# Kernel tuning notes

Hardware: AMD Instinct MI355X
Metric: run time of the kernel (lower is better)

Reference implementation:

```python
import jax, jax.numpy as jnp
import numpy as np

N_NODES = 50000
N_EDGES = 800000
D_IN = 128
HC = 128
D_OUT = 128
BN_EPS = 1e-5
RRELU_SLOPE = (1.0 / 8.0 + 1.0 / 3.0) / 2.0  # RReLU eval mode: (lower+upper)/2 = 11/48


def setup_inputs() -> dict:
    key = jax.random.key(0)
    ks = jax.random.split(key, 10)
    s_in = 1.0 / np.sqrt(D_IN)
    s_hc = 1.0 / np.sqrt(HC)
    return {
        "x": jax.random.normal(ks[0], (N_NODES, D_IN), jnp.float32),
        "edge_index": jax.random.randint(ks[1], (2, N_EDGES), 0, N_NODES),
        "edge_attr": jax.random.uniform(ks[2], (N_EDGES,), jnp.float32),
        # conv1: GraphConv(D_IN -> HC): lin_rel (with bias) + lin_root (no bias)
        "W1_rel": jax.random.normal(ks[3], (HC, D_IN), jnp.float32) * s_in,
        "b1": jnp.zeros((HC,), jnp.float32),
        "W1_root": jax.random.normal(ks[4], (HC, D_IN), jnp.float32) * s_in,
        # bn1 affine params
        "gamma": jnp.ones((HC,), jnp.float32),
        "beta": jnp.zeros((HC,), jnp.float32),
        # conv2: GraphConv(HC -> D_OUT)
        "W2_rel": jax.random.normal(ks[5], (D_OUT, HC), jnp.float32) * s_hc,
        "b2": jnp.zeros((D_OUT,), jnp.float32),
        "W2_root": jax.random.normal(ks[6], (D_OUT, HC), jnp.float32) * s_hc,
    }


def graph_conv(x, src, tgt, edge_w, W_rel, b_rel, W_root):
    # message: edge_weight * x[src]; aggregate: scatter-add into target nodes
    msg = x[src] * edge_w[:, None]                                   # [E, F]
    agg = jax.ops.segment_sum(msg, tgt, num_segments=x.shape[0])     # [N, F]
    return agg @ W_rel.T + b_rel + x @ W_root.T                      # [N, F_out]


def reference(x, edge_index, edge_attr, W1_rel, b1, W1_root, gamma, beta, W2_rel, b2, W2_root):
    src, tgt = edge_index[0], edge_index[1]
    h = graph_conv(x, src, tgt, edge_attr, W1_rel, b1, W1_root)      # [N, HC]
    # BatchNorm1d (training mode: biased batch stats over node dim)
    mean = h.mean(axis=0)
    var = h.var(axis=0)
    h = (h - mean) * jax.lax.rsqrt(var + BN_EPS) * gamma + beta
    # RReLU (deterministic eval slope)
    h = jnp.where(h >= 0, h, h * RRELU_SLOPE)
    return graph_conv(h, src, tgt, edge_attr, W2_rel, b2, W2_root)   # [N, D_OUT]
```

## Files before the change

### kernel.cpp

```cpp
#include <hip/hip_runtime.h>

#define N_NODES 50000
#define N_EDGES 800000
#define F 128
#define BN_EPS 1e-5f
#define SLOPE 0.22916666666666666f

#define NBKT 196
#define BKT_CAP 8192
#define P1_CHUNK 4096
#define P1_EPB 16
#define P1_BLKS 196
#define CASTX_BLKS 6250
#define CASTW_BLKS 64
#define BKT_FINAL_CAP 9984
#define REC_CAP 1160192
#define N_RT 3125
#define NPART 8

typedef __attribute__((ext_vector_type(8))) short bf16x8;
typedef __attribute__((ext_vector_type(4))) float f32x4;
typedef unsigned long long u64;

__device__ __forceinline__ float bf2f(ushort u) {
    union { uint i; float f; } v; v.i = (uint)u << 16; return v.f;
}
__device__ __forceinline__ ushort f2bf(float f) {
    union { float f; uint i; } v; v.f = f;
    uint r = v.i + 0x7fffu + ((v.i >> 16) & 1u);
    return (ushort)(r >> 16);
}
__device__ __forceinline__ uint cvtpk(float lo, float hi) {
    uint r;
    asm("v_cvt_pk_bf16_f32 %0, %1, %2" : "=v"(r) : "v"(lo), "v"(hi));
    return r;
}

__global__ __launch_bounds__(256) void s1p_k(const int* __restrict__ src,
        const int* __restrict__ tgt, const float* __restrict__ ew,
        int* __restrict__ bcur, u64* __restrict__ stg,
        const float* __restrict__ x, ushort* __restrict__ xb,
        const float* __restrict__ W1r, const float* __restrict__ W1t,
        const float* __restrict__ W2r, const float* __restrict__ W2t,
        ushort* __restrict__ wb) {
    const int b = blockIdx.x;
    if (b >= P1_BLKS) {
        if (b < P1_BLKS + CASTX_BLKS) {
            int i = (b - P1_BLKS) * 256 + threadIdx.x;
            float4 v = reinterpret_cast<const float4*>(x)[i];
            ushort4 o;
            o.x = f2bf(v.x); o.y = f2bf(v.y); o.z = f2bf(v.z); o.w = f2bf(v.w);
            reinterpret_cast<ushort4*>(xb)[i] = o;
        } else {
            int i = (b - P1_BLKS - CASTX_BLKS) * 256 + threadIdx.x;
            int m = i >> 12;
            int j = i & 4095;
            const float* sp = (m == 0) ? W1r : (m == 1) ? W1t : (m == 2) ? W2r : W2t;
            float4 v = reinterpret_cast<const float4*>(sp)[j];
            ushort4 o;
            o.x = f2bf(v.x); o.y = f2bf(v.y); o.z = f2bf(v.z); o.w = f2bf(v.w);
            reinterpret_cast<ushort4*>(wb)[i] = o;
        }
        return;
    }
    __shared__ uint cnt[256];
    __shared__ uint base[256];
    __shared__ uint lcur[256];
    __shared__ uint gbase[256];
    __shared__ u64 lrec[P1_CHUNK];

    const int e0 = b * P1_CHUNK;
    const int nE = min(P1_CHUNK, N_EDGES - e0);
    cnt[threadIdx.x] = 0;
    __syncthreads();

    u64 myrec[P1_EPB];
    bool myok[P1_EPB];
#pragma unroll
    for (int k = 0; k < P1_EPB; ++k) {
        int idx = threadIdx.x + (k << 8);
        bool ok = idx < nE;
        myok[k] = ok;
        if (ok) {
            int e = e0 + idx;
            uint t = (uint)tgt[e];
            uint lo = (uint)(ushort)src[e] | ((uint)f2bf(ew[e]) << 16);
            myrec[k] = (u64)lo | ((u64)t << 32);
            atomicAdd(&cnt[t >> 8], 1u);
        }
    }
    __syncthreads();
    uint v = cnt[threadIdx.x];
    base[threadIdx.x] = v;
    __syncthreads();
    for (int o = 1; o < 256; o <<= 1) {
        uint t = (threadIdx.x >= (unsigned)o) ? base[threadIdx.x - o] : 0;
        __syncthreads();
        base[threadIdx.x] += t;
        __syncthreads();
    }
    uint excl = base[threadIdx.x] - v;
    base[threadIdx.x] = excl;
    lcur[threadIdx.x] = excl;
    if (threadIdx.x < NBKT && v > 0)
        gbase[threadIdx.x] = (uint)threadIdx.x * BKT_CAP +
                             (uint)atomicAdd(&bcur[threadIdx.x], (int)v);
    __syncthreads();
#pragma unroll
    for (int k = 0; k < P1_EPB; ++k) {
        if (myok[k]) {
            uint bb = (uint)(myrec[k] >> 40);
            uint slot = atomicAdd(&lcur[bb], 1u);
            lrec[slot] = myrec[k];
        }
    }
    __syncthreads();
    for (int s = threadIdx.x; s < nE; s += 256) {
        u64 r = lrec[s];
        uint bb = (uint)(r >> 40);
        stg[gbase[bb] + ((uint)s - base[bb])] = r;
    }
}

__global__ __launch_bounds__(256) void sort2_k(const int* __restrict__ bcur,
        const u64* __restrict__ stg, uint* __restrict__ recs, int2* __restrict__ rng) {
    __shared__ int lcnt[256];
    __shared__ int lcur[256];
    __shared__ int sc[256];
    __shared__ int fbase_s;
    __shared__ uint lrec[BKT_FINAL_CAP];
    const int b = blockIdx.x;
    const int tid = threadIdx.x;

    int cnt_t = (tid < NBKT) ? bcur[tid] : 0;
    int stride_t = (tid < NBKT) ? (((cnt_t + 7) & ~7) + 1792) : 0;
    sc[tid] = stride_t;
    lcnt[tid] = 0;
    __syncthreads();
    for (int o = 1; o < 256; o <<= 1) {
        int t = (tid >= o) ? sc[tid - o] : 0;
        __syncthreads();
        sc[tid] += t;
        __syncthreads();
    }
    if (tid == b) fbase_s = sc[tid] - stride_t;
    __syncthreads();
    const int fbase = fbase_s;
    const int cnt = bcur[b];
    const u64* sb = stg + (size_t)b * BKT_CAP;

    for (int i = tid; i < cnt; i += 256)
        atomicAdd(&lcnt[(int)(sb[i] >> 32) & 255], 1);
    __syncthreads();
    const int node = b * 256 + tid;
    int myc = lcnt[tid];
    int myp = (myc + 7) & ~7;
    if (node >= N_NODES) myp = 0;
    sc[tid] = myp;
    __syncthreads();
    for (int o = 1; o < 256; o <<= 1) {
        int t = (tid >= o) ? sc[tid - o] : 0;
        __syncthreads();
        sc[tid] += t;
        __syncthreads();
    }
    const int myoff = sc[tid] - myp;
    const int ptot = sc[255];
    lcur[tid] = myoff;
    if (node < N_NODES) rng[node] = make_int2(fbase + myoff, fbase + myoff + myp);
    for (int i = tid; i < ptot; i += 256) lrec[i] = 0;
    __syncthreads();
    for (int i = tid; i < cnt; i += 256) {
        u64 r = sb[i];
        int n = (int)(r >> 32) & 255;
        int p = atomicAdd(&lcur[n], 1);
        lrec[p] = (uint)r;
    }
    __syncthreads();
    for (int i = tid; i < ptot; i += 256) recs[fbase + i] = lrec[i];
}

__device__ __forceinline__ void fma8(float* a, uint4 u, float w) {
    a[0] = fmaf(w, __uint_as_float(u.x << 16), a[0]);
    a[1] = fmaf(w, __uint_as_float(u.x & 0xffff0000u), a[1]);
    a[2] = fmaf(w, __uint_as_float(u.y << 16), a[2]);
    a[3] = fmaf(w, __uint_as_float(u.y & 0xffff0000u), a[3]);
    a[4] = fmaf(w, __uint_as_float(u.z << 16), a[4]);
    a[5] = fmaf(w, __uint_as_float(u.z & 0xffff0000u), a[5]);
    a[6] = fmaf(w, __uint_as_float(u.w << 16), a[6]);
    a[7] = fmaf(w, __uint_as_float(u.w & 0xffff0000u), a[7]);
}

template <int LAYER>
__global__ __launch_bounds__(256) void fused_k(
        const ushort* __restrict__ featb, const int2* __restrict__ rng,
        const uint* __restrict__ recs, const ushort* __restrict__ Wr,
        const ushort* __restrict__ Wt, const float* __restrict__ bias,
        float* __restrict__ Sp, float* __restrict__ S2p,
        ushort* __restrict__ outh, float* __restrict__ outf) {
    __shared__ __align__(16) uint aggu[16 * 64];

    const int tid = threadIdx.x;
    const int lane = tid & 63;
    const int wave = tid >> 6;
    const int row0 = blockIdx.x * 16;
    const int quad = lane >> 4;
    const int l16 = lane & 15;
    const uint fbyte = (uint)l16 << 4;
    const int qq = quad * 2;
    const char* fb = (const char*)featb;

#pragma unroll
    for (int i = 0; i < 4; ++i) {
        const int r = wave * 4 + i;
        const int2 rr = rng[row0 + r];
        float a[8] = {0.f, 0.f, 0.f, 0.f, 0.f, 0.f, 0.f, 0.f};
        for (int p = rr.x; p < rr.y; p += 8) {
            uint2 rc = *reinterpret_cast<const uint2*>(recs + p + qq);
            uint4 u0 = *reinterpret_cast<const uint4*>(fb + (((rc.x & 0xffffu) << 8) + fbyte));
            uint4 u1 = *reinterpret_cast<const uint4*>(fb + (((rc.y & 0xffffu) << 8) + fbyte));
            fma8(a, u0, __uint_as_float(rc.x & 0xffff0000u));
            fma8(a, u1, __uint_as_float(rc.y & 0xffff0000u));
        }
#pragma unroll
        for (int j = 0; j < 8; ++j) {
            a[j] += __shfl_xor(a[j], 16);
            a[j] += __shfl_xor(a[j], 32);
        }
        uint o0 = cvtpk(a[0], a[1]);
        uint o1 = cvtpk(a[2], a[3]);
        uint o2 = cvtpk(a[4], a[5]);
        uint o3 = cvtpk(a[6], a[7]);
        if (lane < 16) {
            const int idx = ((r * 64) + (l16 << 2)) ^ ((r & 7) << 2);
            *reinterpret_cast<uint4*>(&aggu[idx]) = make_uint4(o0, o1, o2, o3);
        }
    }
    __syncthreads();

    const int cb = wave * 32;
    const float bias0 = bias[cb + l16];
    const float bias1 = bias[cb + 16 + l16];

    f32x4 acc0 = {0.f, 0.f, 0.f, 0.f};
    f32x4 acc1 = {0.f, 0.f, 0.f, 0.f};

#pragma unroll
    for (int s = 0; s < 4; ++s) {
        const int k0 = s * 32 + quad * 8;
        const int ai = (l16 * 64 + (k0 >> 1)) ^ ((l16 & 7) << 2);
        bf16x8 aR = *reinterpret_cast<const bf16x8*>(&aggu[ai]);
        bf16x8 w0 = *reinterpret_cast<const bf16x8*>(Wr + (cb + l16) * F + k0);
        bf16x8 w1 = *reinterpret_cast<const bf16x8*>(Wr + (cb + 16 + l16) * F + k0);
        acc0 = __builtin_amdgcn_mfma_f32_16x16x32_bf16(aR, w0, acc0, 0, 0, 0);
        acc1 = __builtin_amdgcn_mfma_f32_16x16x32_bf16(aR, w1, acc1, 0, 0, 0);
    }
#pragma unroll
    for (int s = 0; s < 4; ++s) {
        const int k0 = s * 32 + quad * 8;
        bf16x8 aT = *reinterpret_cast<const bf16x8*>(featb + (size_t)(row0 + l16) * F + k0);
        bf16x8 w0 = *reinterpret_cast<const bf16x8*>(Wt + (cb + l16) * F + k0);
        bf16x8 w1 = *reinterpret_cast<const bf16x8*>(Wt + (cb + 16 + l16) * F + k0);
        acc0 = __builtin_amdgcn_mfma_f32_16x16x32_bf16(aT, w0, acc0, 0, 0, 0);
        acc1 = __builtin_amdgcn_mfma_f32_16x16x32_bf16(aT, w1, acc1, 0, 0, 0);
    }

    const int rbase = row0 + quad * 4;
    if (LAYER == 1) {
        float s0 = 0.f, q0 = 0.f, s1 = 0.f, q1 = 0.f;
#pragma unroll
        for (int g = 0; g < 4; ++g) {
            float v0 = acc0[g] + bias0;
            float v1 = acc1[g] + bias1;
            outh[(size_t)(rbase + g) * F + cb + l16] = f2bf(v0);
            outh[(size_t)(rbase + g) * F + cb + 16 + l16] = f2bf(v1);
            s0 += v0; q0 += v0 * v0;
            s1 += v1; q1 += v1 * v1;
        }
        s0 += __shfl_down(s0, 32); s0 += __shfl_down(s0, 16);
        q0 += __shfl_down(q0, 32); q0 += __shfl_down(q0, 16);
        s1 += __shfl_down(s1, 32); s1 += __shfl_down(s1, 16);
        q1 += __shfl_down(q1, 32); q1 += __shfl_down(q1, 16);
        if (lane < 16) {
            float* Sb = Sp + (size_t)(blockIdx.x & (NPART - 1)) * 128;
            float* S2b = S2p + (size_t)(blockIdx.x & (NPART - 1)) * 128;
            unsafeAtomicAdd(&Sb[cb + lane], s0);
            unsafeAtomicAdd(&S2b[cb + lane], q0);
            unsafeAtomicAdd(&Sb[cb + 16 + lane], s1);
            unsafeAtomicAdd(&S2b[cb + 16 + lane], q1);
        }
    } else {
#pragma unroll
        for (int g = 0; g < 4; ++g) {
            outf[(size_t)(rbase + g) * F + cb + l16] = acc0[g] + bias0;
            outf[(size_t)(rbase + g) * F + cb + 16 + l16] = acc1[g] + bias1;
        }
    }
}

__global__ __launch_bounds__(256) void norm_act_k(const ushort* __restrict__ hraw,
        const float* __restrict__ Sp, const float* __restrict__ S2p,
        const float* __restrict__ gamma, const float* __restrict__ beta,
        ushort* __restrict__ hb) {
    __shared__ float sc_s[128], sh_s[128];
    if (threadIdx.x < 128) {
        int j = threadIdx.x;
        float s = 0.f, q = 0.f;
#pragma unroll
        for (int p = 0; p < NPART; ++p) {
            s += Sp[p * 128 + j];
            q += S2p[p * 128 + j];
        }
        float mean = s * (1.f / N_NODES);
        float var = q * (1.f / N_NODES) - mean * mean;
        float inv = rsqrtf(var + BN_EPS);
        float sc = gamma[j] * inv;
        sc_s[j] = sc;
        sh_s[j] = beta[j] - mean * sc;
    }
    __syncthreads();
    int i = blockIdx.x * 256 + threadIdx.x;
    int cbase = (i & 31) * 4;
    uint2 u = reinterpret_cast<const uint2*>(hraw)[i];
    float4 v = make_float4(bf2f((ushort)u.x), bf2f((ushort)(u.x >> 16)),
                           bf2f((ushort)u.y), bf2f((ushort)(u.y >> 16)));
    float4 sc = *reinterpret_cast<const float4*>(&sc_s[cbase]);
    float4 sh = *reinterpret_cast<const float4*>(&sh_s[cbase]);
    v.x = v.x * sc.x + sh.x;
    v.y = v.y * sc.y + sh.y;
    v.z = v.z * sc.z + sh.z;
    v.w = v.w * sc.w + sh.w;
    v.x = v.x >= 0.f ? v.x : v.x * SLOPE;
    v.y = v.y >= 0.f ? v.y : v.y * SLOPE;
    v.z = v.z >= 0.f ? v.z : v.z * SLOPE;
    v.w = v.w >= 0.f ? v.w : v.w * SLOPE;
    uint2 o;
    o.x = cvtpk(v.x, v.y);
    o.y = cvtpk(v.z, v.w);
    reinterpret_cast<uint2*>(hb)[i] = o;
}

extern "C" void kernel_launch(void* const* d_in, const int* in_sizes, int n_in,
                              void* d_out, int out_size, void* d_ws, size_t ws_size,
                              hipStream_t stream) {
    const float* x     = (const float*)d_in[0];
    const int*   ei    = (const int*)d_in[1];
    const float* ea    = (const float*)d_in[2];
    const float* W1r   = (const float*)d_in[3];
    const float* b1    = (const float*)d_in[4];
    const float* W1t   = (const float*)d_in[5];
    const float* gamma = (const float*)d_in[6];
    const float* beta  = (const float*)d_in[7];
    const float* W2r   = (const float*)d_in[8];
    const float* b2    = (const float*)d_in[9];
    const float* W2t   = (const float*)d_in[10];
    float* out = (float*)d_out;

    char* ws = (char*)d_ws;
    size_t off = 0;
    u64*    stg   = (u64*)(ws + off);    off += (size_t)NBKT * BKT_CAP * 8;
    ushort* featb = (ushort*)(ws + off); off += (size_t)N_NODES * F * 2;
    uint*   recs  = (uint*)(ws + off);   off += (size_t)REC_CAP * 4;
    int*    bcur  = (int*)(ws + off);    off += 256 * 4;
    float*  Sp    = (float*)(ws + off);  off += NPART * 128 * 4;
    float*  S2p   = (float*)(ws + off);  off += NPART * 128 * 4;
    int2*   rng   = (int2*)(ws + off);   off += (size_t)N_NODES * 8;
    ushort* wb    = (ushort*)(ws + off); off += 4 * 16384 * 2;
    ushort* hraw  = (ushort*)stg;

    const int* srcp = ei;
    const int* tgtp = ei + N_EDGES;

    hipMemsetAsync(bcur, 0, 256 * 4 + 2 * NPART * 128 * 4, stream);
    s1p_k<<<P1_BLKS + CASTX_BLKS + CASTW_BLKS, 256, 0, stream>>>(
        srcp, tgtp, ea, bcur, stg, x, featb, W1r, W1t, W2r, W2t, wb);
    sort2_k<<<NBKT, 256, 0, stream>>>(bcur, stg, recs, rng);

    fused_k<1><<<N_RT, 256, 0, stream>>>(featb, rng, recs, wb, wb + 16384, b1,
                                         Sp, S2p, hraw, out);
    norm_act_k<<<CASTX_BLKS, 256, 0, stream>>>(hraw, Sp, S2p, gamma, beta, featb);
    fused_k<2><<<N_RT, 256, 0, stream>>>(featb, rng, recs, wb + 32768, wb + 49152, b2,
                                         Sp, S2p, hraw, out);
}
```

Baseline: 254.8 us.

## Replace two-level bucket sort with global histogram/scan/atomic scatter CSR and interleave gather rows

Replaces the two-pass bucketed edge sort with a plain CSR build: a global per-node degree histogram, a single-block scan that computes padded row ranges, and an atomic-cursor scatter of packed (src, weight) records. The fused aggregation kernel now walks four destination rows together with software-prefetched record loads, which gives more independent feature gathers in flight, and it sets a minimum-occupancy launch bound. The single-block scan serializes across all 50k nodes. The atomic scatter makes the edge order inside each row nondeterministic, so floating-point summation order can vary from run to run. The memset now covers the records buffer, so the padding slots are zero.

```diff
diff --git a/kernel.cpp b/kernel.cpp
--- a/kernel.cpp
+++ b/kernel.cpp
@@ -6,14 +6,10 @@
 #define BN_EPS 1e-5f
 #define SLOPE 0.22916666666666666f
 
-#define NBKT 196
-#define BKT_CAP 8192
-#define P1_CHUNK 4096
-#define P1_EPB 16
-#define P1_BLKS 196
 #define CASTX_BLKS 6250
 #define CASTW_BLKS 64
-#define BKT_FINAL_CAP 9984
+#define HIST_BLKS 782
+#define SCAT_BLKS 782
 #define REC_CAP 1160192
 #define N_RT 3125
 #define NPART 8
@@ -36,23 +32,73 @@
     return r;
 }
 
-__global__ __launch_bounds__(256) void s1p_k(const int* __restrict__ src,
+__global__ __launch_bounds__(256) void hist_k(const int* __restrict__ tgt,
+                                              int* __restrict__ deg) {
+    const int i0 = blockIdx.x * 1024 + threadIdx.x;
+#pragma unroll
+    for (int k = 0; k < 4; ++k) {
+        int i = i0 + (k << 8);
+        if (i < N_EDGES) atomicAdd(&deg[tgt[i]], 1);
+    }
+}
+
+__global__ __launch_bounds__(1024) void scan_k(const int* __restrict__ deg,
+        int* __restrict__ cur, int2* __restrict__ rng) {
+    __shared__ int wsum[16];
+    const int tid = threadIdx.x;
+    const int lane = tid & 63;
+    const int wv = tid >> 6;
+    int carry = 0;
+    for (int base = 0; base < N_NODES; base += 1024) {
+        const int n = base + tid;
+        int d = (n < N_NODES) ? deg[n] : 0;
+        int myp = (d + 7) & ~7;
+        int x = myp;
+#pragma unroll
+        for (int o = 1; o < 64; o <<= 1) {
+            int t = __shfl_up(x, o);
+            if (lane >= o) x += t;
+        }
+        if (lane == 63) wsum[wv] = x;
+        __syncthreads();
+        if (wv == 0 && lane < 16) {
+            int s = wsum[lane];
+#pragma unroll
+            for (int o = 1; o < 16; o <<= 1) {
+                int t = __shfl_up(s, o);
+                if (lane >= o) s += t;
+            }
+            wsum[lane] = s;
+        }
+        __syncthreads();
+        int woff = (wv == 0) ? 0 : wsum[wv - 1];
+        int start = carry + woff + x - myp;
+        if (n < N_NODES) {
+            rng[n] = make_int2(start, start + myp);
+            cur[n] = start;
+        }
+        carry += wsum[15];
+        __syncthreads();
+    }
+}
+
+__global__ __launch_bounds__(256) void scat_k(const int* __restrict__ src,
         const int* __restrict__ tgt, const float* __restrict__ ew,
-        int* __restrict__ bcur, u64* __restrict__ stg,
+        int* __restrict__ cur, uint* __restrict__ recs,
         const float* __restrict__ x, ushort* __restrict__ xb,
         const float* __restrict__ W1r, const float* __restrict__ W1t,
         const float* __restrict__ W2r, const float* __restrict__ W2t,
         ushort* __restrict__ wb) {
     const int b = blockIdx.x;
-    if (b >= P1_BLKS) {
-        if (b < P1_BLKS + CASTX_BLKS) {
-            int i = (b - P1_BLKS) * 256 + threadIdx.x;
+    if (b >= SCAT_BLKS) {
+        if (b < SCAT_BLKS + CASTX_BLKS) {
+            int i = (b - SCAT_BLKS) * 256 + threadIdx.x;
             float4 v = reinterpret_cast<const float4*>(x)[i];
             ushort4 o;
             o.x = f2bf(v.x); o.y = f2bf(v.y); o.z = f2bf(v.z); o.w = f2bf(v.w);
             reinterpret_cast<ushort4*>(xb)[i] = o;
         } else {
-            int i = (b - P1_BLKS - CASTX_BLKS) * 256 + threadIdx.x;
+            int i = (b - SCAT_BLKS - CASTX_BLKS) * 256 + threadIdx.x;
             int m = i >> 12;
             int j = i & 4095;
             const float* sp = (m == 0) ? W1r : (m == 1) ? W1t : (m == 2) ? W2r : W2t;
@@ -63,121 +109,16 @@
         }
         return;
     }
-    __shared__ uint cnt[256];
-    __shared__ uint base[256];
-    __shared__ uint lcur[256];
-    __shared__ uint gbase[256];
-    __shared__ u64 lrec[P1_CHUNK];
-
-    const int e0 = b * P1_CHUNK;
-    const int nE = min(P1_CHUNK, N_EDGES - e0);
-    cnt[threadIdx.x] = 0;
-    __syncthreads();
-
-    u64 myrec[P1_EPB];
-    bool myok[P1_EPB];
-#pragma unroll
-    for (int k = 0; k < P1_EPB; ++k) {
-        int idx = threadIdx.x + (k << 8);
-        bool ok = idx < nE;
-        myok[k] = ok;
-        if (ok) {
-            int e = e0 + idx;
-            uint t = (uint)tgt[e];
-            uint lo = (uint)(ushort)src[e] | ((uint)f2bf(ew[e]) << 16);
-            myrec[k] = (u64)lo | ((u64)t << 32);
-            atomicAdd(&cnt[t >> 8], 1u);
-        }
-    }
-    __syncthreads();
-    uint v = cnt[threadIdx.x];
-    base[threadIdx.x] = v;
-    __syncthreads();
-    for (int o = 1; o < 256; o <<= 1) {
-        uint t = (threadIdx.x >= (unsigned)o) ? base[threadIdx.x - o] : 0;
-        __syncthreads();
-        base[threadIdx.x] += t;
-        __syncthreads();
-    }
-    uint excl = base[threadIdx.x] - v;
-    base[threadIdx.x] = excl;
-    lcur[threadIdx.x] = excl;
-    if (threadIdx.x < NBKT && v > 0)
-        gbase[threadIdx.x] = (uint)threadIdx.x * BKT_CAP +
-                             (uint)atomicAdd(&bcur[threadIdx.x], (int)v);
-    __syncthreads();
-#pragma unroll
-    for (int k = 0; k < P1_EPB; ++k) {
-        if (myok[k]) {
-            uint bb = (uint)(myrec[k] >> 40);
-            uint slot = atomicAdd(&lcur[bb], 1u);
-            lrec[slot] = myrec[k];
-        }
-    }
-    __syncthreads();
-    for (int s = threadIdx.x; s < nE; s += 256) {
-        u64 r = lrec[s];
-        uint bb = (uint)(r >> 40);
-        stg[gbase[bb] + ((uint)s - base[bb])] = r;
-    }
-}
-
-__global__ __launch_bounds__(256) void sort2_k(const int* __restrict__ bcur,
-        const u64* __restrict__ stg, uint* __restrict__ recs, int2* __restrict__ rng) {
-    __shared__ int lcnt[256];
-    __shared__ int lcur[256];
-    __shared__ int sc[256];
-    __shared__ int fbase_s;
-    __shared__ uint lrec[BKT_FINAL_CAP];
-    const int b = blockIdx.x;
-    const int tid = threadIdx.x;
-
-    int cnt_t = (tid < NBKT) ? bcur[tid] : 0;
-    int stride_t = (tid < NBKT) ? (((cnt_t + 7) & ~7) + 1792) : 0;
-    sc[tid] = stride_t;
-    lcnt[tid] = 0;
-    __syncthreads();
-    for (int o = 1; o < 256; o <<= 1) {
-        int t = (tid >= o) ? sc[tid - o] : 0;
-        __syncthreads();
-        sc[tid] += t;
-        __syncthreads();
-    }
-    if (tid == b) fbase_s = sc[tid] - stride_t;
-    __syncthreads();
-    const int fbase = fbase_s;
-    const int cnt = bcur[b];
-    const u64* sb = stg + (size_t)b * BKT_CAP;
-
-    for (int i = tid; i < cnt; i += 256)
-        atomicAdd(&lcnt[(int)(sb[i] >> 32) & 255], 1);
-    __syncthreads();
-    const int node = b * 256 + tid;
-    int myc = lcnt[tid];
-    int myp = (myc + 7) & ~7;
-    if (node >= N_NODES) myp = 0;
-    sc[tid] = myp;
-    __syncthreads();
-    for (int o = 1; o < 256; o <<= 1) {
-        int t = (tid >= o) ? sc[tid - o] : 0;
-        __syncthreads();
-        sc[tid] += t;
-        __syncthreads();
-    }
-    const int myoff = sc[tid] - myp;
-    const int ptot = sc[255];
-    lcur[tid] = myoff;
-    if (node < N_NODES) rng[node] = make_int2(fbase + myoff, fbase + myoff + myp);
-    for (int i = tid; i < ptot; i += 256) lrec[i] = 0;
-    __syncthreads();
-    for (int i = tid; i < cnt; i += 256) {
-        u64 r = sb[i];
-        int n = (int)(r >> 32) & 255;
-        int p = atomicAdd(&lcur[n], 1);
-        lrec[p] = (uint)r;
-    }
-    __syncthreads();
-    for (int i = tid; i < ptot; i += 256) recs[fbase + i] = lrec[i];
+    const int i0 = b * 1024 + threadIdx.x;
+#pragma unroll
+    for (int k = 0; k < 4; ++k) {
+        int i = i0 + (k << 8);
+        if (i < N_EDGES) {
+            uint rec = (uint)(ushort)src[i] | ((uint)f2bf(ew[i]) << 16);
+            int pos = atomicAdd(&cur[tgt[i]], 1);
+            recs[pos] = rec;
+        }
+    }
 }
 
 __device__ __forceinline__ void fma8(float* a, uint4 u, float w) {
@@ -191,8 +132,11 @@
     a[7] = fmaf(w, __uint_as_float(u.w & 0xffff0000u), a[7]);
 }
 
+#define FEAT(r) (*reinterpret_cast<const uint4*>(fb + ((((r) & 0xffffu) << 8) + fbyte)))
+#define WHI(r) __uint_as_float((r) & 0xffff0000u)
+
 template <int LAYER>
-__global__ __launch_bounds__(256) void fused_k(
+__global__ __launch_bounds__(256, 4) void fused_k(
         const ushort* __restrict__ featb, const int2* __restrict__ rng,
         const uint* __restrict__ recs, const ushort* __restrict__ Wr,
         const ushort* __restrict__ Wt, const float* __restrict__ bias,
@@ -210,31 +154,68 @@
     const int qq = quad * 2;
     const char* fb = (const char*)featb;
 
-#pragma unroll
-    for (int i = 0; i < 4; ++i) {
-        const int r = wave * 4 + i;
-        const int2 rr = rng[row0 + r];
-        float a[8] = {0.f, 0.f, 0.f, 0.f, 0.f, 0.f, 0.f, 0.f};
-        for (int p = rr.x; p < rr.y; p += 8) {
-            uint2 rc = *reinterpret_cast<const uint2*>(recs + p + qq);
-            uint4 u0 = *reinterpret_cast<const uint4*>(fb + (((rc.x & 0xffffu) << 8) + fbyte));
-            uint4 u1 = *reinterpret_cast<const uint4*>(fb + (((rc.y & 0xffffu) << 8) + fbyte));
-            fma8(a, u0, __uint_as_float(rc.x & 0xffff0000u));
-            fma8(a, u1, __uint_as_float(rc.y & 0xffff0000u));
-        }
-#pragma unroll
-        for (int j = 0; j < 8; ++j) {
-            a[j] += __shfl_xor(a[j], 16);
-            a[j] += __shfl_xor(a[j], 32);
-        }
-        uint o0 = cvtpk(a[0], a[1]);
-        uint o1 = cvtpk(a[2], a[3]);
-        uint o2 = cvtpk(a[4], a[5]);
-        uint o3 = cvtpk(a[6], a[7]);
-        if (lane < 16) {
-            const int idx = ((r * 64) + (l16 << 2)) ^ ((r & 7) << 2);
-            *reinterpret_cast<uint4*>(&aggu[idx]) = make_uint4(o0, o1, o2, o3);
-        }
+    const int nb = row0 + wave * 4;
+    int2 r0 = rng[nb + 0], r1 = rng[nb + 1], r2 = rng[nb + 2], r3 = rng[nb + 3];
+    int p0 = __builtin_amdgcn_readfirstlane(r0.x), e0 = __builtin_amdgcn_readfirstlane(r0.y);
+    int p1 = __builtin_amdgcn_readfirstlane(r1.x), e1 = __builtin_amdgcn_readfirstlane(r1.y);
+    int p2 = __builtin_amdgcn_readfirstlane(r2.x), e2 = __builtin_amdgcn_readfirstlane(r2.y);
+    int p3 = __builtin_amdgcn_readfirstlane(r3.x), e3 = __builtin_amdgcn_readfirstlane(r3.y);
+
+    float a0[8] = {0.f,0.f,0.f,0.f,0.f,0.f,0.f,0.f};
+    float a1[8] = {0.f,0.f,0.f,0.f,0.f,0.f,0.f,0.f};
+    float a2[8] = {0.f,0.f,0.f,0.f,0.f,0.f,0.f,0.f};
+    float a3[8] = {0.f,0.f,0.f,0.f,0.f,0.f,0.f,0.f};
+
+    bool g0 = p0 < e0, g1 = p1 < e1, g2 = p2 < e2, g3 = p3 < e3;
+    uint2 rc0, rc1, rc2, rc3;
+    if (g0) rc0 = *reinterpret_cast<const uint2*>(recs + p0 + qq);
+    if (g1) rc1 = *reinterpret_cast<const uint2*>(recs + p1 + qq);
+    if (g2) rc2 = *reinterpret_cast<const uint2*>(recs + p2 + qq);
+    if (g3) rc3 = *reinterpret_cast<const uint2*>(recs + p3 + qq);
+
+    while (g0 | g1 | g2 | g3) {
+        uint4 u00, u01, u10, u11, u20, u21, u30, u31;
+        if (g0) { u00 = FEAT(rc0.x); u01 = FEAT(rc0.y); }
+        if (g1) { u10 = FEAT(rc1.x); u11 = FEAT(rc1.y); }
+        if (g2) { u20 = FEAT(rc2.x); u21 = FEAT(rc2.y); }
+        if (g3) { u30 = FEAT(rc3.x); u31 = FEAT(rc3.y); }
+        p0 += 8; p1 += 8; p2 += 8; p3 += 8;
+        bool h0 = g0 & (p0 < e0), h1 = g1 & (p1 < e1);
+        bool h2 = g2 & (p2 < e2), h3 = g3 & (p3 < e3);
+        uint2 rn0, rn1, rn2, rn3;
+        if (h0) rn0 = *reinterpret_cast<const uint2*>(recs + p0 + qq);
+        if (h1) rn1 = *reinterpret_cast<const uint2*>(recs + p1 + qq);
+        if (h2) rn2 = *reinterpret_cast<const uint2*>(recs + p2 + qq);
+        if (h3) rn3 = *reinterpret_cast<const uint2*>(recs + p3 + qq);
+        if (g0) { fma8(a0, u00, WHI(rc0.x)); fma8(a0, u01, WHI(rc0.y)); }
+        if (g1) { fma8(a1, u10, WHI(rc1.x)); fma8(a1, u11, WHI(rc1.y)); }
+        if (g2) { fma8(a2, u20, WHI(rc2.x)); fma8(a2, u21, WHI(rc2.y)); }
+        if (g3) { fma8(a3, u30, WHI(rc3.x)); fma8(a3, u31, WHI(rc3.y)); }
+        rc0 = rn0; rc1 = rn1; rc2 = rn2; rc3 = rn3;
+        g0 = h0; g1 = h1; g2 = h2; g3 = h3;
+    }
+
+#pragma unroll
+    for (int j = 0; j < 8; ++j) {
+        a0[j] += __shfl_xor(a0[j], 16); a0[j] += __shfl_xor(a0[j], 32);
+        a1[j] += __shfl_xor(a1[j], 16); a1[j] += __shfl_xor(a1[j], 32);
+        a2[j] += __shfl_xor(a2[j], 16); a2[j] += __shfl_xor(a2[j], 32);
+        a3[j] += __shfl_xor(a3[j], 16); a3[j] += __shfl_xor(a3[j], 32);
+    }
+    if (lane < 16) {
+        const int rr = wave * 4;
+        int i0 = ((rr + 0) * 64 + (l16 << 2)) ^ (((rr + 0) & 7) << 2);
+        int i1 = ((rr + 1) * 64 + (l16 << 2)) ^ (((rr + 1) & 7) << 2);
+        int i2 = ((rr + 2) * 64 + (l16 << 2)) ^ (((rr + 2) & 7) << 2);
+        int i3 = ((rr + 3) * 64 + (l16 << 2)) ^ (((rr + 3) & 7) << 2);
+        *reinterpret_cast<uint4*>(&aggu[i0]) =
+            make_uint4(cvtpk(a0[0],a0[1]), cvtpk(a0[2],a0[3]), cvtpk(a0[4],a0[5]), cvtpk(a0[6],a0[7]));
+        *reinterpret_cast<uint4*>(&aggu[i1]) =
+            make_uint4(cvtpk(a1[0],a1[1]), cvtpk(a1[2],a1[3]), cvtpk(a1[4],a1[5]), cvtpk(a1[6],a1[7]));
+        *reinterpret_cast<uint4*>(&aggu[i2]) =
+            make_uint4(cvtpk(a2[0],a2[1]), cvtpk(a2[2],a2[3]), cvtpk(a2[4],a2[5]), cvtpk(a2[6],a2[7]));
+        *reinterpret_cast<uint4*>(&aggu[i3]) =
+            make_uint4(cvtpk(a3[0],a3[1]), cvtpk(a3[2],a3[3]), cvtpk(a3[4],a3[5]), cvtpk(a3[6],a3[7]));
     }
     __syncthreads();
 
@@ -358,23 +339,26 @@
 
     char* ws = (char*)d_ws;
     size_t off = 0;
-    u64*    stg   = (u64*)(ws + off);    off += (size_t)NBKT * BKT_CAP * 8;
     ushort* featb = (ushort*)(ws + off); off += (size_t)N_NODES * F * 2;
+    ushort* hraw  = (ushort*)(ws + off); off += (size_t)N_NODES * F * 2;
+    int2*   rng   = (int2*)(ws + off);   off += (size_t)N_NODES * 8;
+    int*    cur   = (int*)(ws + off);    off += (size_t)N_NODES * 4;
+    ushort* wb    = (ushort*)(ws + off); off += 4 * 16384 * 2;
+    char*   zbase = ws + off;
     uint*   recs  = (uint*)(ws + off);   off += (size_t)REC_CAP * 4;
-    int*    bcur  = (int*)(ws + off);    off += 256 * 4;
+    int*    deg   = (int*)(ws + off);    off += (size_t)N_NODES * 4;
     float*  Sp    = (float*)(ws + off);  off += NPART * 128 * 4;
     float*  S2p   = (float*)(ws + off);  off += NPART * 128 * 4;
-    int2*   rng   = (int2*)(ws + off);   off += (size_t)N_NODES * 8;
-    ushort* wb    = (ushort*)(ws + off); off += 4 * 16384 * 2;
-    ushort* hraw  = (ushort*)stg;
+    size_t  zlen  = (size_t)(ws + off - zbase);
 
     const int* srcp = ei;
     const int* tgtp = ei + N_EDGES;
 
-    hipMemsetAsync(bcur, 0, 256 * 4 + 2 * NPART * 128 * 4, stream);
-    s1p_k<<<P1_BLKS + CASTX_BLKS + CASTW_BLKS, 256, 0, stream>>>(
-        srcp, tgtp, ea, bcur, stg, x, featb, W1r, W1t, W2r, W2t, wb);
-    sort2_k<<<NBKT, 256, 0, stream>>>(bcur, stg, recs, rng);
+    hipMemsetAsync(zbase, 0, zlen, stream);
+    hist_k<<<HIST_BLKS, 256, 0, stream>>>(tgtp, deg);
+    scan_k<<<1, 1024, 0, stream>>>(deg, cur, rng);
+    scat_k<<<SCAT_BLKS + CASTX_BLKS + CASTW_BLKS, 256, 0, stream>>>(
+        srcp, tgtp, ea, cur, recs, x, featb, W1r, W1t, W2r, W2t, wb);
 
     fused_k<1><<<N_RT, 256, 0, stream>>>(featb, rng, recs, wb, wb + 16384, b1,
                                          Sp, S2p, hraw, out);
```

Result: slower. 370.9 us (+45.5%).
